# Performance work log

Measured on AMD Instinct MI355X. Metric: run time of the kernel, lower is better.

## Reference

```python
import jax, jax.numpy as jnp
import numpy as np

IS_DECODER = True
NEG = -100000.0


def setup_inputs() -> dict:
    key = jax.random.key(0)
    ks = jax.random.split(key, 8)
    B, S, E, H = 8, 2048, 1024, 64
    return {
        "hidden_state": jax.random.normal(ks[0], (B, S, E), dtype=jnp.float32),
        "attention_masks": jax.random.randint(ks[1], (B, S), 0, 2, dtype=jnp.int32),
        "Wq": jax.random.normal(ks[2], (E, H), dtype=jnp.float32) / np.sqrt(E),
        "bq": jax.random.normal(ks[3], (H,), dtype=jnp.float32) * 0.02,
        "Wk": jax.random.normal(ks[4], (E, H), dtype=jnp.float32) / np.sqrt(E),
        "bk": jax.random.normal(ks[5], (H,), dtype=jnp.float32) * 0.02,
        "Wv": jax.random.normal(ks[6], (E, H), dtype=jnp.float32) / np.sqrt(E),
        "bv": jax.random.normal(ks[7], (H,), dtype=jnp.float32) * 0.02,
    }


def reference(hidden_state, attention_masks, Wq, bq, Wk, bk, Wv, bv):
    # projections: q,k,v [B,S,H]
    q = hidden_state @ Wq + bq
    k = hidden_state @ Wk + bk
    v = hidden_state @ Wv + bv
    dim = q.shape[-1]
    # scores [B,S,S]
    score = jnp.einsum("bqh,bkh->bqk", q, k) / jnp.sqrt(jnp.float32(dim))
    m = attention_masks.astype(score.dtype)  # [B,S]
    pad = 1.0 - m
    amm = m[:, :, None] * m[:, None, :]      # [B,S,S]
    pmm = pad[:, :, None] * pad[:, None, :]
    if IS_DECODER:
        S = m.shape[-1]
        amm = amm * jnp.tril(jnp.ones((S, S), dtype=score.dtype))
    coupling = 1.0 - amm - pmm
    score = score + coupling * NEG
    weights = jax.nn.softmax(score, axis=-1)
    return jnp.einsum("bqk,bkh->bqh", weights, v)
```

## Files before the change

kernel.cpp:

```cpp
#include <hip/hip_runtime.h>

typedef float f32x4 __attribute__((ext_vector_type(4)));
typedef float f32x16 __attribute__((ext_vector_type(16)));
typedef unsigned int u32x4 __attribute__((ext_vector_type(4)));
typedef __bf16 bf16x8 __attribute__((ext_vector_type(8)));
typedef unsigned short ushort_t;

#define NEG2 (-144269.5f)
#define SCLQ (0.18033688f)

constexpr int Ss = 2048, Ee = 1024, Hh = 64;

static __device__ __forceinline__ ushort_t f2bfu(float f) {
  return __builtin_bit_cast(ushort_t, (__bf16)f);
}
static __device__ __forceinline__ f32x4 mfma16(bf16x8 a, bf16x8 b, f32x4 c) {
  return __builtin_amdgcn_mfma_f32_16x16x32_bf16(a, b, c, 0, 0, 0);
}
static __device__ __forceinline__ f32x16 mfma32(bf16x8 a, bf16x8 b, f32x16 c) {
  return __builtin_amdgcn_mfma_f32_32x32x16_bf16(a, b, c, 0, 0, 0);
}
static __device__ __forceinline__ unsigned cvtpk(float a, float b) {
  unsigned r;
  asm("v_cvt_pk_bf16_f32 %0, %1, %2" : "=v"(r) : "v"(a), "v"(b));
  return r;
}
static __device__ __forceinline__ void swap32(unsigned& a, unsigned& b) {
  asm("v_permlane32_swap_b32 %0, %1" : "+v"(a), "+v"(b));
}
static __device__ __forceinline__ void gload_lds16(const void* g, void* l) {
  __builtin_amdgcn_global_load_lds(
      (const __attribute__((address_space(1))) unsigned int*)g,
      (__attribute__((address_space(3))) unsigned int*)l, 16, 0, 0);
}


__global__ __launch_bounds__(256) void k_wtrans(const float* __restrict__ Wq,
                                                const float* __restrict__ Wk,
                                                const float* __restrict__ Wv,
                                                ushort_t* __restrict__ Wsw) {
  __shared__ float tile[64][65];
  const float* W = (blockIdx.y == 0) ? Wq : (blockIdx.y == 1 ? Wk : Wv);
  int kt = blockIdx.x, t = threadIdx.x;
  int r = t >> 2, cq = t & 3;
  const float* src = W + (kt * 64 + r) * Hh + cq * 16;
#pragma unroll
  for (int j = 0; j < 16; j += 4) {
    float4 v = *reinterpret_cast<const float4*>(src + j);
    tile[r][cq * 16 + j + 0] = v.x;
    tile[r][cq * 16 + j + 1] = v.y;
    tile[r][cq * 16 + j + 2] = v.z;
    tile[r][cq * 16 + j + 3] = v.w;
  }
  __syncthreads();
  int n = t >> 2, kq = t & 3;
  int rr = blockIdx.y * 64 + n;
  ushort_t ob[16];
#pragma unroll
  for (int j = 0; j < 16; ++j) ob[j] = f2bfu(tile[kq * 16 + j][n]);
#pragma unroll
  for (int j = 0; j < 2; ++j) {
    int c16 = 2 * kq + j;
    size_t off = ((size_t)(kt * 192 + rr)) * 64 + (size_t)(((c16 ^ (rr & 7))) * 8);
    *reinterpret_cast<uint4*>(Wsw + off) = reinterpret_cast<uint4*>(ob)[j];
  }
}

__global__ __launch_bounds__(256, 2) void k_proj(const float* __restrict__ hs,
                                                 const float* __restrict__ bq,
                                                 const float* __restrict__ bk,
                                                 const float* __restrict__ bv,
                                                 const ushort_t* __restrict__ Wsw,
                                                 const int* __restrict__ am,
                                                 ushort_t* __restrict__ qf_,
                                                 ushort_t* __restrict__ kf_,
                                                 ushort_t* __restrict__ vf_,
                                                 float* __restrict__ pen) {
  __shared__ __align__(16) ushort_t bufA[2][32][72];
  __shared__ __align__(16) ushort_t bufW[2][192 * 64];

  int t = threadIdx.x, w = t >> 6, l = t & 63, g = l >> 4, c = l & 15;
  int wm = w >> 1, wn = w & 1;
  int row0 = blockIdx.x * 32;

  int ar = t >> 3, ach = t & 7;
  const float* agp = hs + (size_t)(row0 + ar) * Ee + ach * 8;

  f32x4 acc[6];
#pragma unroll
  for (int nt = 0; nt < 6; ++nt) acc[nt] = f32x4{0.f, 0.f, 0.f, 0.f};
  float4 aR0, aR1;

  auto LOADA = [&](int kk) {
    aR0 = *reinterpret_cast<const float4*>(agp + kk);
    aR1 = *reinterpret_cast<const float4*>(agp + kk + 4);
  };
  auto WRITEA = [&](int buf) {
    bf16x8 av;
    av[0] = (__bf16)aR0.x; av[1] = (__bf16)aR0.y; av[2] = (__bf16)aR0.z; av[3] = (__bf16)aR0.w;
    av[4] = (__bf16)aR1.x; av[5] = (__bf16)aR1.y; av[6] = (__bf16)aR1.z; av[7] = (__bf16)aR1.w;
    *reinterpret_cast<bf16x8*>(&bufA[buf][ar][ach * 8]) = av;
  };
  auto GLW = [&](int buf, int s) {
    const ushort_t* base = Wsw + (size_t)s * 12288;
#pragma unroll
    for (int j = 0; j < 6; ++j) {
      int seg = j * 4 + w;
      const ushort_t* gp = base + seg * 512 + l * 8;
      gload_lds16(gp, &bufW[buf][seg * 512]);
    }
  };
  auto COMPUTE = [&](int buf) {
    const ushort_t* Ab = &bufA[buf][wm * 16 + c][0];
    bf16x8 af0 = *reinterpret_cast<const bf16x8*>(Ab + g * 8);
    bf16x8 af1 = *reinterpret_cast<const bf16x8*>(Ab + 32 + g * 8);
#pragma unroll
    for (int nt = 0; nt < 6; ++nt) {
      int r = wn * 96 + nt * 16 + c;
      int slot = g ^ (r & 7);
      const ushort_t* Wb = &bufW[buf][r * 64];
      bf16x8 b0 = *reinterpret_cast<const bf16x8*>(Wb + slot * 8);
      bf16x8 b1 = *reinterpret_cast<const bf16x8*>(Wb + (slot ^ 4) * 8);
      acc[nt] = mfma16(af0, b0, acc[nt]);
      acc[nt] = mfma16(af1, b1, acc[nt]);
    }
  };

  LOADA(0);
  WRITEA(0);
  GLW(0, 0);
  LOADA(64);
  __builtin_amdgcn_sched_barrier(0);

  int cur = 0;
  for (int s = 0; s < 16; ++s) {
    __syncthreads();
    if (s < 15) {
      WRITEA(cur ^ 1);
      GLW(cur ^ 1, s + 1);
    }
    if (s < 14) {
      LOADA((s + 2) * 64);
      __builtin_amdgcn_sched_barrier(0);
    }
    COMPUTE(cur);
    cur ^= 1;
  }

#pragma unroll
  for (int nt = 0; nt < 6; ++nt) {
    int T = wn * 6 + nt;
    int m = T >> 2;
    int h = (T & 3) * 16 + c;
    const float* bias = (m == 0) ? bq : ((m == 1) ? bk : bv);
    float bb = bias[h];
    int cc = h >> 4, hh = (h >> 3) & 1, jj = h & 7;
    int dt = h >> 5, dl = h & 31;
#pragma unroll
    for (int i = 0; i < 4; ++i) {
      int row = row0 + wm * 16 + g * 4 + i;
      float val = acc[nt][i] + bb;
      int bi = row >> 11, rl = row & 2047;
      if (m == 0) {
        size_t a = ((((size_t)(bi * 64 + (rl >> 5)) * 4 + cc) * 2 + hh) * 32 + (rl & 31)) * 8 + jj;
        qf_[a] = f2bfu(val * SCLQ);
      } else if (m == 1) {
        size_t a = ((((size_t)(bi * 64 + (rl >> 5)) * 4 + cc) * 2 + hh) * 32 + (rl & 31)) * 8 + jj;
        kf_[a] = f2bfu(val);
      } else {
        int s16 = rl >> 4, vh = (rl >> 3) & 1, vj = rl & 7;
        size_t a = ((((size_t)(bi * 128 + s16) * 2 + dt) * 2 + vh) * 32 + dl) * 8 + vj;
        vf_[a] = f2bfu(val);
      }
    }
  }

  if (t < 32) {
    int grow = row0 + t;
    int bi = grow >> 11, s2 = grow & 2047;
    int mv = am[grow];
    pen[((size_t)bi * 2 + 0) * Ss + s2] = mv ? 0.f : NEG2;
    pen[((size_t)bi * 2 + 1) * Ss + s2] = mv ? NEG2 : 0.f;
  }
}

__global__ __launch_bounds__(256, 3) void k_attn(const ushort_t* __restrict__ qs,
                                                 const ushort_t* __restrict__ km,
                                                 const ushort_t* __restrict__ vm,
                                                 const int* __restrict__ am,
                                                 const float* __restrict__ pen,
                                                 float* __restrict__ opart,
                                                 float* __restrict__ lpart) {
  __shared__ float obuf[4][32][68];
  __shared__ float lls[4][32];

  int t = threadIdx.x, w = t >> 6, l = t & 63, lo = l & 31, hi = l >> 5;
  int bid = blockIdx.x;
  int b = bid & 7, qt = (bid >> 3) & 63, kh = bid >> 9;
  int q0 = qt * 32;

  const size_t laneoff = (size_t)hi * 256 + lo * 8;

  const ushort_t* qbase = qs + (size_t)(b * 64 + qt) * 2048 + laneoff;
  bf16x8 qf[4];
#pragma unroll
  for (int c = 0; c < 4; ++c)
    qf[c] = *reinterpret_cast<const bf16x8*>(qbase + (size_t)c * 512);

  int mq = am[b * Ss + q0 + lo];
  float negq = mq ? NEG2 : 0.f;
  const float* psel = pen + ((size_t)b * 2 + (mq ? 0 : 1)) * Ss;

  float ll = 0.f;
  f32x16 o0 = {0.f, 0.f, 0.f, 0.f, 0.f, 0.f, 0.f, 0.f, 0.f, 0.f, 0.f, 0.f, 0.f, 0.f, 0.f, 0.f};
  f32x16 o1 = o0;
  const f32x16 z16 = o0;

  const int kvbeg = kh * 1024 + w * 256;
  const ushort_t* kb = km + (size_t)b * 131072 + laneoff;
  const ushort_t* vb = vm + (size_t)b * 131072 + laneoff;

  for (int it = 0; it < 8; ++it) {
    const int kv0 = kvbeg + it * 32;
    const int kt32 = kv0 >> 5, s16 = kv0 >> 4;

    const ushort_t* kfp = kb + (size_t)kt32 * 2048;
    bf16x8 kf0 = *reinterpret_cast<const bf16x8*>(kfp);
    bf16x8 kf1 = *reinterpret_cast<const bf16x8*>(kfp + 512);
    bf16x8 kf2 = *reinterpret_cast<const bf16x8*>(kfp + 1024);
    bf16x8 kf3 = *reinterpret_cast<const bf16x8*>(kfp + 1536);
    const ushort_t* vfp = vb + (size_t)s16 * 1024;
    bf16x8 vf00 = *reinterpret_cast<const bf16x8*>(vfp);
    bf16x8 vf01 = *reinterpret_cast<const bf16x8*>(vfp + 512);
    bf16x8 vf10 = *reinterpret_cast<const bf16x8*>(vfp + 1024);
    bf16x8 vf11 = *reinterpret_cast<const bf16x8*>(vfp + 1536);

    f32x4 pv[4];
#pragma unroll
    for (int j = 0; j < 4; ++j)
      pv[j] = *reinterpret_cast<const f32x4*>(psel + kv0 + j * 8 + hi * 4);

    f32x16 sc = mfma32(kf0, qf[0], z16);
    sc = mfma32(kf1, qf[1], sc);
    sc = mfma32(kf2, qf[2], sc);
    sc = mfma32(kf3, qf[3], sc);

    if (kv0 == q0) {
#pragma unroll
      for (int r = 0; r < 16; ++r) {
        int kr = (r & 3) + 8 * (r >> 2) + 4 * hi;
        sc[r] += pv[r >> 2][r & 3] + ((kr > lo) ? negq : 0.f);
      }
    } else {
      float addt = (kv0 > q0) ? negq : 0.f;
#pragma unroll
      for (int r = 0; r < 16; ++r) sc[r] += pv[r >> 2][r & 3] + addt;
    }

    float p[16], ts = 0.f;
#pragma unroll
    for (int r = 0; r < 16; ++r) {
      p[r] = __builtin_amdgcn_exp2f(sc[r]);
      ts += p[r];
    }
    ll += ts;

    unsigned x0 = cvtpk(p[0], p[1]), y0 = cvtpk(p[2], p[3]);
    unsigned z0 = cvtpk(p[4], p[5]), w0 = cvtpk(p[6], p[7]);
    swap32(x0, z0);
    swap32(y0, w0);
    unsigned x1 = cvtpk(p[8], p[9]), y1 = cvtpk(p[10], p[11]);
    unsigned z1 = cvtpk(p[12], p[13]), w1 = cvtpk(p[14], p[15]);
    swap32(x1, z1);
    swap32(y1, w1);
    bf16x8 pa0 = __builtin_bit_cast(bf16x8, u32x4{x0, y0, z0, w0});
    bf16x8 pa1 = __builtin_bit_cast(bf16x8, u32x4{x1, y1, z1, w1});

    o0 = mfma32(pa0, vf00, o0);
    o0 = mfma32(pa1, vf10, o0);
    o1 = mfma32(pa0, vf01, o1);
    o1 = mfma32(pa1, vf11, o1);
  }

  ll += __shfl_xor(ll, 32);

#pragma unroll
  for (int r = 0; r < 16; ++r) {
    int qrow = (r & 3) + 8 * (r >> 2) + 4 * hi;
    obuf[w][qrow][lo] = o0[r];
    obuf[w][qrow][32 + lo] = o1[r];
  }
  if (hi == 0) lls[w][lo] = ll;
  __syncthreads();

  int qr = t >> 3, dg = t & 7;
  float lg = lls[0][qr] + lls[1][qr] + lls[2][qr] + lls[3][qr];
  float a8[8] = {0.f, 0.f, 0.f, 0.f, 0.f, 0.f, 0.f, 0.f};
#pragma unroll
  for (int ww = 0; ww < 4; ++ww) {
    float4 c0 = *reinterpret_cast<const float4*>(&obuf[ww][qr][dg * 8]);
    float4 c1 = *reinterpret_cast<const float4*>(&obuf[ww][qr][dg * 8 + 4]);
    a8[0] += c0.x; a8[1] += c0.y; a8[2] += c0.z; a8[3] += c0.w;
    a8[4] += c1.x; a8[5] += c1.y; a8[6] += c1.z; a8[7] += c1.w;
  }
  float* op = opart + (((size_t)kh * 8 + b) * Ss + q0 + qr) * 64 + dg * 8;
  float4 r0v = {a8[0], a8[1], a8[2], a8[3]};
  float4 r1v = {a8[4], a8[5], a8[6], a8[7]};
  *reinterpret_cast<float4*>(op) = r0v;
  *reinterpret_cast<float4*>(op + 4) = r1v;
  if (dg == 0) lpart[((size_t)kh * 8 + b) * Ss + q0 + qr] = lg;
}

__global__ __launch_bounds__(256) void k_fin(const float* __restrict__ op,
                                             const float* __restrict__ lp,
                                             float* __restrict__ out) {
  int gi = blockIdx.x * 256 + threadIdx.x;
  int row = gi >> 4;
  float lsum = lp[row] + lp[row + 16384];
  f32x4 a = reinterpret_cast<const f32x4*>(op)[gi];
  f32x4 b = reinterpret_cast<const f32x4*>(op)[gi + 262144];
  float inv = 1.f / lsum;
  f32x4 r = (a + b) * inv;
  reinterpret_cast<f32x4*>(out)[gi] = r;
}

extern "C" void kernel_launch(void* const* d_in, const int* in_sizes, int n_in,
                              void* d_out, int out_size, void* d_ws, size_t ws_size,
                              hipStream_t stream) {
  const float* hs = (const float*)d_in[0];
  const int* am = (const int*)d_in[1];
  const float* Wq = (const float*)d_in[2];
  const float* bq = (const float*)d_in[3];
  const float* Wk = (const float*)d_in[4];
  const float* bk = (const float*)d_in[5];
  const float* Wv = (const float*)d_in[6];
  const float* bv = (const float*)d_in[7];
  float* out = (float*)d_out;

  char* ws = (char*)d_ws;
  ushort_t* qsp = (ushort_t*)(ws + 0);
  ushort_t* kp = (ushort_t*)(ws + (2u << 20));
  ushort_t* vtp = (ushort_t*)(ws + (4u << 20));
  ushort_t* wtp = (ushort_t*)(ws + (6u << 20));
  float* penp = (float*)(ws + (6u << 20) + (512u << 10));
  float* opart = (float*)(ws + (8u << 20));
  float* lpart = (float*)(ws + (16u << 20));

  k_wtrans<<<dim3(16, 3), 256, 0, stream>>>(Wq, Wk, Wv, wtp);
  k_proj<<<dim3(512), 256, 0, stream>>>(hs, bq, bk, bv, wtp, am, qsp, kp, vtp, penp);
  k_attn<<<dim3(1024), 256, 0, stream>>>(qsp, kp, vtp, am, penp, opart, lpart);
  k_fin<<<dim3(1024), 256, 0, stream>>>(opart, lpart, out);
}
```

Baseline: 52.65 us.

## Process two query tiles per attention block to reuse K/V fragments

Each attention block now handles 64 query rows (two 32-row tiles) instead of 32, so every K and V fragment loaded from global memory feeds two sets of MFMAs. The grid is halved to 512 blocks and launch bounds drop to 2 waves per SIMD to make room for the extra accumulators and Q fragments, while the shared reduction buffer doubles. The aim is to halve K/V load traffic per unit of work. The cost is lower occupancy and fewer blocks, which can reduce latency hiding on a GPU with many CUs.

```diff
diff --git a/kernel.cpp b/kernel.cpp
--- a/kernel.cpp
+++ b/kernel.cpp
@@ -184,37 +184,41 @@
   }
 }
 
-__global__ __launch_bounds__(256, 3) void k_attn(const ushort_t* __restrict__ qs,
+__global__ __launch_bounds__(256, 2) void k_attn(const ushort_t* __restrict__ qs,
                                                  const ushort_t* __restrict__ km,
                                                  const ushort_t* __restrict__ vm,
                                                  const int* __restrict__ am,
                                                  const float* __restrict__ pen,
                                                  float* __restrict__ opart,
                                                  float* __restrict__ lpart) {
-  __shared__ float obuf[4][32][68];
-  __shared__ float lls[4][32];
+  __shared__ float obuf[4][64][68];
+  __shared__ float lls[4][64];
 
   int t = threadIdx.x, w = t >> 6, l = t & 63, lo = l & 31, hi = l >> 5;
   int bid = blockIdx.x;
-  int b = bid & 7, qt = (bid >> 3) & 63, kh = bid >> 9;
-  int q0 = qt * 32;
+  int b = bid & 7, qt2 = (bid >> 3) & 31, kh = bid >> 8;
+  int q0A = qt2 * 64, q0B = q0A + 32;
 
   const size_t laneoff = (size_t)hi * 256 + lo * 8;
 
-  const ushort_t* qbase = qs + (size_t)(b * 64 + qt) * 2048 + laneoff;
-  bf16x8 qf[4];
-#pragma unroll
-  for (int c = 0; c < 4; ++c)
-    qf[c] = *reinterpret_cast<const bf16x8*>(qbase + (size_t)c * 512);
-
-  int mq = am[b * Ss + q0 + lo];
-  float negq = mq ? NEG2 : 0.f;
-  const float* psel = pen + ((size_t)b * 2 + (mq ? 0 : 1)) * Ss;
-
-  float ll = 0.f;
-  f32x16 o0 = {0.f, 0.f, 0.f, 0.f, 0.f, 0.f, 0.f, 0.f, 0.f, 0.f, 0.f, 0.f, 0.f, 0.f, 0.f, 0.f};
-  f32x16 o1 = o0;
-  const f32x16 z16 = o0;
+  const ushort_t* qbaseA = qs + (size_t)(b * 64 + qt2 * 2) * 2048 + laneoff;
+  const ushort_t* qbaseB = qbaseA + 2048;
+  bf16x8 qfA[4], qfB[4];
+#pragma unroll
+  for (int c = 0; c < 4; ++c) {
+    qfA[c] = *reinterpret_cast<const bf16x8*>(qbaseA + (size_t)c * 512);
+    qfB[c] = *reinterpret_cast<const bf16x8*>(qbaseB + (size_t)c * 512);
+  }
+
+  int mqA = am[b * Ss + q0A + lo], mqB = am[b * Ss + q0B + lo];
+  float negqA = mqA ? NEG2 : 0.f, negqB = mqB ? NEG2 : 0.f;
+  const float* pselA = pen + ((size_t)b * 2 + (mqA ? 0 : 1)) * Ss;
+  const float* pselB = pen + ((size_t)b * 2 + (mqB ? 0 : 1)) * Ss;
+
+  float llA = 0.f, llB = 0.f;
+  f32x16 o0A = {0.f, 0.f, 0.f, 0.f, 0.f, 0.f, 0.f, 0.f, 0.f, 0.f, 0.f, 0.f, 0.f, 0.f, 0.f, 0.f};
+  f32x16 o1A = o0A, o0B = o0A, o1B = o0A;
+  const f32x16 z16 = o0A;
 
   const int kvbeg = kh * 1024 + w * 256;
   const ushort_t* kb = km + (size_t)b * 131072 + laneoff;
@@ -235,80 +239,129 @@
     bf16x8 vf10 = *reinterpret_cast<const bf16x8*>(vfp + 1024);
     bf16x8 vf11 = *reinterpret_cast<const bf16x8*>(vfp + 1536);
 
-    f32x4 pv[4];
+    f32x4 pvA[4];
 #pragma unroll
     for (int j = 0; j < 4; ++j)
-      pv[j] = *reinterpret_cast<const f32x4*>(psel + kv0 + j * 8 + hi * 4);
-
-    f32x16 sc = mfma32(kf0, qf[0], z16);
-    sc = mfma32(kf1, qf[1], sc);
-    sc = mfma32(kf2, qf[2], sc);
-    sc = mfma32(kf3, qf[3], sc);
-
-    if (kv0 == q0) {
+      pvA[j] = *reinterpret_cast<const f32x4*>(pselA + kv0 + j * 8 + hi * 4);
+
+    f32x16 scA = mfma32(kf0, qfA[0], z16);
+    scA = mfma32(kf1, qfA[1], scA);
+    scA = mfma32(kf2, qfA[2], scA);
+    scA = mfma32(kf3, qfA[3], scA);
+    f32x16 scB = mfma32(kf0, qfB[0], z16);
+    scB = mfma32(kf1, qfB[1], scB);
+    scB = mfma32(kf2, qfB[2], scB);
+    scB = mfma32(kf3, qfB[3], scB);
+
+    if (kv0 == q0A) {
 #pragma unroll
       for (int r = 0; r < 16; ++r) {
         int kr = (r & 3) + 8 * (r >> 2) + 4 * hi;
-        sc[r] += pv[r >> 2][r & 3] + ((kr > lo) ? negq : 0.f);
+        scA[r] += pvA[r >> 2][r & 3] + ((kr > lo) ? negqA : 0.f);
       }
     } else {
-      float addt = (kv0 > q0) ? negq : 0.f;
-#pragma unroll
-      for (int r = 0; r < 16; ++r) sc[r] += pv[r >> 2][r & 3] + addt;
-    }
-
-    float p[16], ts = 0.f;
+      float addt = (kv0 > q0A) ? negqA : 0.f;
+#pragma unroll
+      for (int r = 0; r < 16; ++r) scA[r] += pvA[r >> 2][r & 3] + addt;
+    }
+    float pA[16], tsA = 0.f;
 #pragma unroll
     for (int r = 0; r < 16; ++r) {
-      p[r] = __builtin_amdgcn_exp2f(sc[r]);
-      ts += p[r];
-    }
-    ll += ts;
-
-    unsigned x0 = cvtpk(p[0], p[1]), y0 = cvtpk(p[2], p[3]);
-    unsigned z0 = cvtpk(p[4], p[5]), w0 = cvtpk(p[6], p[7]);
-    swap32(x0, z0);
-    swap32(y0, w0);
-    unsigned x1 = cvtpk(p[8], p[9]), y1 = cvtpk(p[10], p[11]);
-    unsigned z1 = cvtpk(p[12], p[13]), w1 = cvtpk(p[14], p[15]);
-    swap32(x1, z1);
-    swap32(y1, w1);
-    bf16x8 pa0 = __builtin_bit_cast(bf16x8, u32x4{x0, y0, z0, w0});
-    bf16x8 pa1 = __builtin_bit_cast(bf16x8, u32x4{x1, y1, z1, w1});
-
-    o0 = mfma32(pa0, vf00, o0);
-    o0 = mfma32(pa1, vf10, o0);
-    o1 = mfma32(pa0, vf01, o1);
-    o1 = mfma32(pa1, vf11, o1);
-  }
-
-  ll += __shfl_xor(ll, 32);
+      pA[r] = __builtin_amdgcn_exp2f(scA[r]);
+      tsA += pA[r];
+    }
+    llA += tsA;
+    unsigned xa0 = cvtpk(pA[0], pA[1]), ya0 = cvtpk(pA[2], pA[3]);
+    unsigned za0 = cvtpk(pA[4], pA[5]), wa0 = cvtpk(pA[6], pA[7]);
+    swap32(xa0, za0);
+    swap32(ya0, wa0);
+    unsigned xa1 = cvtpk(pA[8], pA[9]), ya1 = cvtpk(pA[10], pA[11]);
+    unsigned za1 = cvtpk(pA[12], pA[13]), wa1 = cvtpk(pA[14], pA[15]);
+    swap32(xa1, za1);
+    swap32(ya1, wa1);
+    bf16x8 paA0 = __builtin_bit_cast(bf16x8, u32x4{xa0, ya0, za0, wa0});
+    bf16x8 paA1 = __builtin_bit_cast(bf16x8, u32x4{xa1, ya1, za1, wa1});
+    o0A = mfma32(paA0, vf00, o0A);
+    o0A = mfma32(paA1, vf10, o0A);
+    o1A = mfma32(paA0, vf01, o1A);
+    o1A = mfma32(paA1, vf11, o1A);
+
+    f32x4 pvB[4];
+#pragma unroll
+    for (int j = 0; j < 4; ++j)
+      pvB[j] = *reinterpret_cast<const f32x4*>(pselB + kv0 + j * 8 + hi * 4);
+
+    if (kv0 == q0B) {
+#pragma unroll
+      for (int r = 0; r < 16; ++r) {
+        int kr = (r & 3) + 8 * (r >> 2) + 4 * hi;
+        scB[r] += pvB[r >> 2][r & 3] + ((kr > lo) ? negqB : 0.f);
+      }
+    } else {
+      float addt = (kv0 > q0B) ? negqB : 0.f;
+#pragma unroll
+      for (int r = 0; r < 16; ++r) scB[r] += pvB[r >> 2][r & 3] + addt;
+    }
+    float pB[16], tsB = 0.f;
+#pragma unroll
+    for (int r = 0; r < 16; ++r) {
+      pB[r] = __builtin_amdgcn_exp2f(scB[r]);
+      tsB += pB[r];
+    }
+    llB += tsB;
+    unsigned xb0 = cvtpk(pB[0], pB[1]), yb0 = cvtpk(pB[2], pB[3]);
+    unsigned zb0 = cvtpk(pB[4], pB[5]), wb0 = cvtpk(pB[6], pB[7]);
+    swap32(xb0, zb0);
+    swap32(yb0, wb0);
+    unsigned xb1 = cvtpk(pB[8], pB[9]), yb1 = cvtpk(pB[10], pB[11]);
+    unsigned zb1 = cvtpk(pB[12], pB[13]), wb1 = cvtpk(pB[14], pB[15]);
+    swap32(xb1, zb1);
+    swap32(yb1, wb1);
+    bf16x8 paB0 = __builtin_bit_cast(bf16x8, u32x4{xb0, yb0, zb0, wb0});
+    bf16x8 paB1 = __builtin_bit_cast(bf16x8, u32x4{xb1, yb1, zb1, wb1});
+    o0B = mfma32(paB0, vf00, o0B);
+    o0B = mfma32(paB1, vf10, o0B);
+    o1B = mfma32(paB0, vf01, o1B);
+    o1B = mfma32(paB1, vf11, o1B);
+  }
+
+  llA += __shfl_xor(llA, 32);
+  llB += __shfl_xor(llB, 32);
 
 #pragma unroll
   for (int r = 0; r < 16; ++r) {
     int qrow = (r & 3) + 8 * (r >> 2) + 4 * hi;
-    obuf[w][qrow][lo] = o0[r];
-    obuf[w][qrow][32 + lo] = o1[r];
-  }
-  if (hi == 0) lls[w][lo] = ll;
+    obuf[w][qrow][lo] = o0A[r];
+    obuf[w][qrow][32 + lo] = o1A[r];
+    obuf[w][32 + qrow][lo] = o0B[r];
+    obuf[w][32 + qrow][32 + lo] = o1B[r];
+  }
+  if (hi == 0) {
+    lls[w][lo] = llA;
+    lls[w][32 + lo] = llB;
+  }
   __syncthreads();
 
   int qr = t >> 3, dg = t & 7;
-  float lg = lls[0][qr] + lls[1][qr] + lls[2][qr] + lls[3][qr];
-  float a8[8] = {0.f, 0.f, 0.f, 0.f, 0.f, 0.f, 0.f, 0.f};
-#pragma unroll
-  for (int ww = 0; ww < 4; ++ww) {
-    float4 c0 = *reinterpret_cast<const float4*>(&obuf[ww][qr][dg * 8]);
-    float4 c1 = *reinterpret_cast<const float4*>(&obuf[ww][qr][dg * 8 + 4]);
-    a8[0] += c0.x; a8[1] += c0.y; a8[2] += c0.z; a8[3] += c0.w;
-    a8[4] += c1.x; a8[5] += c1.y; a8[6] += c1.z; a8[7] += c1.w;
-  }
-  float* op = opart + (((size_t)kh * 8 + b) * Ss + q0 + qr) * 64 + dg * 8;
-  float4 r0v = {a8[0], a8[1], a8[2], a8[3]};
-  float4 r1v = {a8[4], a8[5], a8[6], a8[7]};
-  *reinterpret_cast<float4*>(op) = r0v;
-  *reinterpret_cast<float4*>(op + 4) = r1v;
-  if (dg == 0) lpart[((size_t)kh * 8 + b) * Ss + q0 + qr] = lg;
+#pragma unroll
+  for (int pass = 0; pass < 2; ++pass) {
+    int row = pass * 32 + qr;
+    float lg = lls[0][row] + lls[1][row] + lls[2][row] + lls[3][row];
+    float a8[8] = {0.f, 0.f, 0.f, 0.f, 0.f, 0.f, 0.f, 0.f};
+#pragma unroll
+    for (int ww = 0; ww < 4; ++ww) {
+      float4 c0 = *reinterpret_cast<const float4*>(&obuf[ww][row][dg * 8]);
+      float4 c1 = *reinterpret_cast<const float4*>(&obuf[ww][row][dg * 8 + 4]);
+      a8[0] += c0.x; a8[1] += c0.y; a8[2] += c0.z; a8[3] += c0.w;
+      a8[4] += c1.x; a8[5] += c1.y; a8[6] += c1.z; a8[7] += c1.w;
+    }
+    float* op = opart + (((size_t)kh * 8 + b) * Ss + q0A + row) * 64 + dg * 8;
+    float4 r0v = {a8[0], a8[1], a8[2], a8[3]};
+    float4 r1v = {a8[4], a8[5], a8[6], a8[7]};
+    *reinterpret_cast<float4*>(op) = r0v;
+    *reinterpret_cast<float4*>(op + 4) = r1v;
+    if (dg == 0) lpart[((size_t)kh * 8 + b) * Ss + q0A + row] = lg;
+  }
 }
 
 __global__ __launch_bounds__(256) void k_fin(const float* __restrict__ op,
@@ -348,6 +401,6 @@
 
   k_wtrans<<<dim3(16, 3), 256, 0, stream>>>(Wq, Wk, Wv, wtp);
   k_proj<<<dim3(512), 256, 0, stream>>>(hs, bq, bk, bv, wtp, am, qsp, kp, vtp, penp);
-  k_attn<<<dim3(1024), 256, 0, stream>>>(qsp, kp, vtp, am, penp, opart, lpart);
+  k_attn<<<dim3(512), 256, 0, stream>>>(qsp, kp, vtp, am, penp, opart, lpart);
   k_fin<<<dim3(1024), 256, 0, stream>>>(opart, lpart, out);
 }
```

After: 47.36 us. 1.11x faster.
